# Kernel optimization log

Hardware: AMD Instinct MI355X
Metric: run time of the kernel (lower is better)

## Reference

```python
import jax, jax.numpy as jnp
import numpy as np

N = 100000   # nodes
E = 1600000  # edges
G = 1000     # graphs
S = 32       # state_dim
H = 128      # hidden_dim_message / hidden_dim_output
F = 1        # num_features (edge coulomb)
ROUNDS = 5
NEG_SLOPE = 0.01
LN_EPS = 1e-5


def _ln(x, g, b):
    m = jnp.mean(x, axis=-1, keepdims=True)
    v = jnp.var(x, axis=-1, keepdims=True)
    return (x - m) / jnp.sqrt(v + LN_EPS) * g + b


def _lrelu(x):
    return jnp.where(x >= 0, x, NEG_SLOPE * x)


def _kaiming(k, shape):
    # torch kaiming_normal_(mode='fan_out', nonlinearity='leaky_relu'); W stored [in,out]
    gain = np.sqrt(2.0 / (1.0 + NEG_SLOPE ** 2))
    std = gain / np.sqrt(shape[1])
    return jax.random.normal(k, shape, dtype=jnp.float32) * std


def setup_inputs() -> dict:
    key = jax.random.key(0)
    ks = jax.random.split(key, 10)
    return {
        'node_from': jax.random.randint(ks[0], (E,), 0, N),
        'node_to': jax.random.randint(ks[1], (E,), 0, N),
        'edge_coulomb': jax.random.normal(ks[2], (E, F), dtype=jnp.float32),
        'node_graph_index': jax.random.randint(ks[3], (N,), 0, G),
        'num_nodes': N,
        'num_graphs': G,
        # message_net params
        'W1': _kaiming(ks[4], (S + F, H)), 'b1': jnp.zeros((H,), jnp.float32),
        'g1': jnp.ones((H,), jnp.float32), 'be1': jnp.zeros((H,), jnp.float32),
        'W2': _kaiming(ks[5], (H, S)), 'b2': jnp.zeros((S,), jnp.float32),
        'g2': jnp.ones((S,), jnp.float32), 'be2': jnp.zeros((S,), jnp.float32),
        # output_net params
        'Wo1': _kaiming(ks[6], (S, H)), 'bo1': jnp.zeros((H,), jnp.float32),
        'go': jnp.ones((H,), jnp.float32), 'beo': jnp.zeros((H,), jnp.float32),
        'Wo2': _kaiming(ks[7], (H, 2)), 'bo2': jnp.zeros((2,), jnp.float32),
    }


def reference(node_from, node_to, edge_coulomb, node_graph_index, num_nodes, num_graphs,
              W1, b1, g1, be1, W2, b2, g2, be2, Wo1, bo1, go, beo, Wo2, bo2):
    state = jnp.zeros((num_nodes, S), dtype=edge_coulomb.dtype)
    for _ in range(ROUNDS):
        inp = jnp.concatenate([state[node_from], edge_coulomb], axis=1)  # [E, S+F]
        h = _lrelu(_ln(inp @ W1 + b1, g1, be1))                           # [E, H]
        msg = _lrelu(_ln(h @ W2 + b2, g2, be2))                           # [E, S]
        state = state + jax.ops.segment_sum(msg, node_to, num_segments=num_nodes)
    graph_state = jax.ops.segment_sum(state, node_graph_index, num_segments=num_graphs)  # [G, S]
    h = _lrelu(_ln(graph_state @ Wo1 + bo1, go, beo))
    ev = h @ Wo2 + bo2                                                    # [G, 2]
    mu = ev[:, :1]
    var = jax.nn.softplus(ev[:, 1:])
    return jnp.concatenate([mu, var], axis=1)
```

## Files before the change

kernel.cpp:

```cpp
#include <hip/hip_runtime.h>
#include <hip/hip_bf16.h>

#define NN 100000
#define NE 1600000
#define NG 1000
#define SS 32
#define HH 128
#define ROUNDS 5

constexpr float NEG = 0.01f;
constexpr float EPS = 1e-5f;

constexpr long al4(long x)  { return (x + 3) & ~3L; }
constexpr long al16(long x) { return (x + 15) & ~15L; }

constexpr long OFF_STATE = 0;
constexpr long OFF_GS    = OFF_STATE + (long)NN * SS;
constexpr long OFF_W1T   = OFF_GS + (long)NG * SS;
constexpr long OFF_B1    = OFF_W1T + HH * 33;
constexpr long OFF_G1    = OFF_B1 + HH;
constexpr long OFF_BE1   = OFF_G1 + HH;
constexpr long OFF_W2    = OFF_BE1 + HH;
constexpr long OFF_B2    = OFF_W2 + HH * SS;
constexpr long OFF_G2    = OFF_B2 + SS;
constexpr long OFF_BE2   = OFF_G2 + SS;
constexpr long OFF_WO1   = OFF_BE2 + SS;
constexpr long OFF_BO1   = OFF_WO1 + SS * HH;
constexpr long OFF_GO    = OFF_BO1 + HH;
constexpr long OFF_BEO   = OFF_GO + HH;
constexpr long OFF_WO2   = OFF_BEO + HH;
constexpr long OFF_BO2   = OFF_WO2 + HH * 2;
constexpr long OFF_W1L   = al4(OFF_BO2 + 2);
constexpr long OFF_WSC   = OFF_W1L + HH;
constexpr long OFF_W1B   = al4(OFF_WSC + 2);
constexpr long OFF_W2F   = OFF_W1B + 2048;
constexpr long OFF_WPK   = OFF_W2F + 2048;
constexpr long OFF_Z0P   = OFF_WPK + 192;
constexpr long W_END     = OFF_Z0P + 68;
constexpr long OFF_DELTA = al4(W_END);
constexpr long F_Z      = al4(W_END);
constexpr long F_DEG    = al4(F_Z + (long)NN * 68);
constexpr long F_START  = F_DEG + NN;
constexpr long F_CURSOR = F_START + NN + 4;
constexpr long F_SDEG   = F_CURSOR + NN;
constexpr long F_SSTART = F_SDEG + NN;
constexpr long F_SCUR   = F_SSTART + NN + 4;
constexpr long F_BSUM   = F_SCUR + NN;
constexpr long F_GDEG   = F_BSUM + 512;
constexpr long F_GSTART = F_GDEG + NG;
constexpr long F_GCUR   = F_GSTART + NG + 4;
constexpr long F_GLIST  = F_GCUR + NG;
constexpr long F_EPK    = al16(F_GLIST + NN);
constexpr long F_MSG    = al16(F_EPK + (long)NE * 4);
constexpr long F_RC     = F_MSG;
constexpr long WS_TOTAL = F_MSG + (long)NE * 16;
constexpr long WS_FALLBACK = OFF_DELTA + (long)NN * SS;
constexpr int  NBLK_N  = (NN + 255) / 256;
constexpr int  CHSHIFT = 18;
constexpr int  NCH     = (NE + (1 << CHSHIFT) - 1) >> CHSHIFT;

typedef float f32x4 __attribute__((ext_vector_type(4)));
typedef unsigned int u32x4 __attribute__((ext_vector_type(4)));
typedef short s16x8 __attribute__((ext_vector_type(8)));

__device__ __forceinline__ s16x8 as_s16x8(u32x4 u) {
    union { u32x4 a; s16x8 b; } c; c.a = u; return c.b;
}
__device__ __forceinline__ float bf2f(unsigned short u) {
    union { unsigned int i; float f; } v;
    v.i = ((unsigned int)u) << 16;
    return v.f;
}
__device__ __forceinline__ float lo_bf(unsigned int p) {
    union { unsigned int i; float f; } v; v.i = p << 16; return v.f;
}
__device__ __forceinline__ float hi_bf(unsigned int p) {
    union { unsigned int i; float f; } v; v.i = p & 0xFFFF0000u; return v.f;
}
__device__ __forceinline__ unsigned short f2bf(float f) {
    union { float f; unsigned int u; } x; x.f = f;
    return (unsigned short)((x.u + 0x7FFFu + ((x.u >> 16) & 1u)) >> 16);
}
__device__ __forceinline__ unsigned int pack_bf2(float a, float b) {
    return (unsigned int)f2bf(a) | ((unsigned int)f2bf(b) << 16);
}
#if defined(__has_builtin)
#if __has_builtin(__builtin_amdgcn_cvt_pk_bf16_f32)
#define HAVE_CVT_PK_BF16 1
#endif
#endif
__device__ __forceinline__ unsigned int cvt2bf(float a, float b) {
#ifdef HAVE_CVT_PK_BF16
    auto r = __builtin_amdgcn_cvt_pk_bf16_f32(a, b);
    unsigned int u; __builtin_memcpy(&u, &r, 4); return u;
#else
    return pack_bf2(a, b);
#endif
}
template <int CTRL>
__device__ __forceinline__ float ror_add(float x) {
    int v = __builtin_amdgcn_update_dpp(0, __float_as_int(x), CTRL, 0xF, 0xF, true);
    return x + __int_as_float(v);
}
__device__ __forceinline__ float row_reduce16(float x) {
    x = ror_add<0x121>(x);
    x = ror_add<0x122>(x);
    x = ror_add<0x124>(x);
    x = ror_add<0x128>(x);
    return x;
}
__device__ __forceinline__ int is_bf16(const void* g1raw) {
    return (((const unsigned int*)g1raw)[0] & 0xFFFFu) != 0u;
}
__device__ __forceinline__ float ldf(const void* p, long idx, int bf) {
    return bf ? bf2f(((const unsigned short*)p)[idx]) : ((const float*)p)[idx];
}

__global__ void prep_kernel(
    const void* __restrict__ W1,  const void* __restrict__ b1,
    const void* __restrict__ g1,  const void* __restrict__ be1,
    const void* __restrict__ W2,  const void* __restrict__ b2,
    const void* __restrict__ g2,  const void* __restrict__ be2,
    const void* __restrict__ Wo1, const void* __restrict__ bo1,
    const void* __restrict__ go,  const void* __restrict__ beo,
    const void* __restrict__ Wo2, const void* __restrict__ bo2,
    float* __restrict__ ws)
{
    const int bf = is_bf16(g1);
    long idx = (long)blockIdx.x * blockDim.x + threadIdx.x;
    if (idx < (long)NN * SS) { ws[OFF_STATE + idx] = 0.f; ws[OFF_DELTA + idx] = 0.f; }
    if (idx < (long)NG * SS) ws[OFF_GS + idx] = 0.f;
    if (idx < NN) { ((int*)(ws + F_DEG))[idx] = 0; ((int*)(ws + F_SDEG))[idx] = 0; }
    if (idx < NG) ((int*)(ws + F_GDEG))[idx] = 0;
    if (idx < 33 * HH) {
        int i = (int)(idx / HH), k = (int)(idx % HH);
        ws[OFF_W1T + (long)k * 33 + i] = ldf(W1, idx, bf);
    }
    if (idx < HH) {
        ws[OFF_B1  + idx] = ldf(b1,  idx, bf);
        ws[OFF_G1  + idx] = ldf(g1,  idx, bf);
        ws[OFF_BE1 + idx] = ldf(be1, idx, bf);
        ws[OFF_BO1 + idx] = ldf(bo1, idx, bf);
        ws[OFF_GO  + idx] = ldf(go,  idx, bf);
        ws[OFF_BEO + idx] = ldf(beo, idx, bf);
        ws[OFF_W1L + idx] = ldf(W1, (long)32 * HH + idx, bf);
    }
    if (idx == 0) {
        float sw = 0.f, sq = 0.f;
        float sb = 0.f, qb = 0.f, db = 0.f;
        for (int i = 0; i < HH; i++) {
            float w = ldf(W1, (long)32 * HH + i, bf);
            float x = ldf(b1, i, bf);
            sw += w; sq = fmaf(w, w, sq);
            sb += x; qb = fmaf(x, x, qb); db = fmaf(x, w, db);
        }
        ws[OFF_WSC] = sw; ws[OFF_WSC + 1] = sq;
        float* z0s = ws + OFF_Z0P + 64;
        z0s[0] = sb; z0s[1] = qb; z0s[2] = db; z0s[3] = 0.f;
    }
    if (idx < 64) {
        ((unsigned int*)(ws + OFF_Z0P))[idx] =
            cvt2bf(ldf(b1, 2 * idx, bf), ldf(b1, 2 * idx + 1, bf));
    }
    if (idx < HH * SS) ws[OFF_W2 + idx] = ldf(W2, idx, bf);
    if (idx < SS) {
        ws[OFF_B2  + idx] = ldf(b2,  idx, bf);
        ws[OFF_G2  + idx] = ldf(g2,  idx, bf);
        ws[OFF_BE2 + idx] = ldf(be2, idx, bf);
    }
    if (idx < SS * HH) ws[OFF_WO1 + idx] = ldf(Wo1, idx, bf);
    if (idx < HH * 2)  ws[OFF_WO2 + idx] = ldf(Wo2, idx, bf);
    if (idx < 2)       ws[OFF_BO2 + idx] = ldf(bo2, idx, bf);
    if (idx < 2048) {
        int w = (int)idx;
        int qq = w & 3, L = (w >> 2) & 63, t = (int)(w >> 8);
        int k0 = (L >> 4) * 8 + 2 * qq;
        int n  = t * 16 + (L & 15);
        ((unsigned int*)(ws + OFF_W1B))[w] =
            pack_bf2(ldf(W1, (long)k0 * HH + n, bf), ldf(W1, (long)(k0 + 1) * HH + n, bf));
    }
    if (idx < 2048) {
        int w = (int)idx;
        int qq = w & 3, L = (w >> 2) & 63, t2 = (w >> 8) & 1, ks = (int)(w >> 9);
        int k0 = ks * 32 + (L >> 4) * 8 + 2 * qq;
        int n  = t2 * 16 + (L & 15);
        float v0 = ldf(W2, (long)k0 * SS + n, bf);
        float v1 = ldf(W2, (long)(k0 + 1) * SS + n, bf);
        ((unsigned int*)(ws + OFF_W2F))[w] = pack_bf2(v0, v1);
    }
    if (idx < 192) {
        int w = (int)idx;
        int grp = w / 12, rem = w % 12, slot = rem >> 2, q = rem & 3;
        int ks = grp >> 2, quad = grp & 3;
        int n = ks * 32 + quad * 8 + 2 * q;
        float v0, v1;
        if (slot == 0)      { v0 = ldf(W1, (long)32 * HH + n, bf); v1 = ldf(W1, (long)32 * HH + n + 1, bf); }
        else if (slot == 1) { v0 = ldf(g1, n, bf);  v1 = ldf(g1, n + 1, bf); }
        else                { v0 = ldf(be1, n, bf); v1 = ldf(be1, n + 1, bf); }
        ((unsigned int*)(ws + OFF_WPK))[w] = pack_bf2(v0, v1);
    }
}

__global__ void hist2_kernel(const int* __restrict__ nto, const int* __restrict__ nfrom,
                             float* ws) {
    int e = blockIdx.x * 256 + threadIdx.x;
    if (e < NE) {
        atomicAdd(&((int*)(ws + F_DEG))[nto[e]], 1);
        atomicAdd(&((int*)(ws + F_SDEG))[nfrom[e]], 1);
    }
}

__global__ void scan1_kernel(float* ws, long degOff, long startOff) {
    __shared__ int sh[256];
    int* deg   = (int*)(ws + degOff);
    int* start = (int*)(ws + startOff);
    int* bsum  = (int*)(ws + F_BSUM);
    int i = blockIdx.x * 256 + threadIdx.x;
    int x = (i < NN) ? deg[i] : 0;
    sh[threadIdx.x] = x;
    __syncthreads();
    for (int off = 1; off < 256; off <<= 1) {
        int t = (threadIdx.x >= off) ? sh[threadIdx.x - off] : 0;
        __syncthreads();
        sh[threadIdx.x] += t;
        __syncthreads();
    }
    int incl = sh[threadIdx.x];
    if (i < NN) start[i] = incl - x;
    if (threadIdx.x == 255) bsum[blockIdx.x] = incl;
}

__global__ void scan2p_kernel(float* ws) {
    __shared__ int sh[512];
    int* bsum = (int*)(ws + F_BSUM);
    int t = threadIdx.x;
    int x = (t < NBLK_N) ? bsum[t] : 0;
    sh[t] = x;
    __syncthreads();
    for (int off = 1; off < 512; off <<= 1) {
        int v = (t >= off) ? sh[t - off] : 0;
        __syncthreads();
        sh[t] += v;
        __syncthreads();
    }
    if (t < NBLK_N) bsum[t] = sh[t] - x;
}

__global__ void scan3_kernel(float* ws, long startOff, long curOff) {
    int* start  = (int*)(ws + startOff);
    int* cursor = (int*)(ws + curOff);
    int* bsum   = (int*)(ws + F_BSUM);
    int i = blockIdx.x * 256 + threadIdx.x;
    if (i < NN) {
        int s = start[i] + bsum[i >> 8];
        start[i] = s;
        cursor[i] = s;
        if (i == 0) start[NN] = NE;
    }
}

__global__ void fillseq_kernel(const int* __restrict__ nfrom, const int* __restrict__ nto,
                               const void* __restrict__ ec, const void* __restrict__ g1raw,
                               float* ws) {
    int e = blockIdx.x * 256 + threadIdx.x;
    if (e < NE) {
        int u = nfrom[e];
        int v = nto[e];
        float ecv = ldf(ec, e, is_bf16(g1raw));
        int dpos = atomicAdd(&((int*)(ws + F_CURSOR))[v], 1);
        int spos = atomicAdd(&((int*)(ws + F_SCUR))[u], 1);
        union { float f; unsigned int i; } c; c.f = ecv;
        u32x4 o; o[0] = (unsigned int)u; o[1] = c.i; o[2] = (unsigned int)dpos; o[3] = (unsigned int)spos;
        *(u32x4*)((unsigned int*)(ws + F_RC) + (long)e * 4) = o;
    }
}

__global__ void fillsc_kernel(float* ws, int chunk) {
    int e = blockIdx.x * 256 + threadIdx.x;
    if (e < NE) {
        u32x4 rc = *(const u32x4*)((const unsigned int*)(ws + F_RC) + (long)e * 4);
        if ((int)(rc[3] >> CHSHIFT) == chunk) {
            u32x4 o; o[0] = rc[0]; o[1] = rc[1]; o[2] = rc[2]; o[3] = 0u;
            *(u32x4*)((unsigned int*)(ws + F_EPK) + (long)rc[3] * 4) = o;
        }
    }
}

__global__ void ghist_kernel(const int* __restrict__ gidx, float* ws) {
    int i = blockIdx.x * 256 + threadIdx.x;
    if (i < NN) atomicAdd(&((int*)(ws + F_GDEG))[gidx[i]], 1);
}

__global__ void gscan_kernel(float* ws) {
    __shared__ int sh[1024];
    int* deg   = (int*)(ws + F_GDEG);
    int* start = (int*)(ws + F_GSTART);
    int* cur   = (int*)(ws + F_GCUR);
    int t = threadIdx.x;
    int x = (t < NG) ? deg[t] : 0;
    sh[t] = x;
    __syncthreads();
    for (int off = 1; off < 1024; off <<= 1) {
        int v = (t >= off) ? sh[t - off] : 0;
        __syncthreads();
        sh[t] += v;
        __syncthreads();
    }
    if (t < NG) { start[t] = sh[t] - x; cur[t] = sh[t] - x; }
    if (t == 0) start[NG] = NN;
}

__global__ void gfill_kernel(const int* __restrict__ gidx, float* ws) {
    int i = blockIdx.x * 256 + threadIdx.x;
    if (i < NN) {
        int pos = atomicAdd(&((int*)(ws + F_GCUR))[gidx[i]], 1);
        ((int*)(ws + F_GLIST))[pos] = i;
    }
}

__global__ void z0_kernel(float* __restrict__ ws)
{
    long idx = (long)blockIdx.x * 256 + threadIdx.x;
    if (idx < (long)NN * 68) {
        int slot = (int)(idx % 68);
        ((unsigned int*)(ws + F_Z))[idx] = ((const unsigned int*)(ws + OFF_Z0P))[slot];
    }
}

__launch_bounds__(256)
__global__ void node_kernel(float* __restrict__ ws, int do_z)
{
    __shared__ unsigned short zl[4][16 * 136];
    __shared__ float stl[64 * 33];
    const long nbase = (long)blockIdx.x * 64;

    {
        int t = threadIdx.x;
        int vl = t >> 2, sub = t & 3;
        long v = nbase + vl;
        if (v < NN) {
            const int* start = (const int*)(ws + F_START);
            const u32x4* mb = (const u32x4*)(ws + F_MSG);
            int s0 = start[v], s1 = start[v + 1];
            float* st = ws + OFF_STATE + v * SS + sub * 8;
            float a0 = st[0], a1 = st[1], a2 = st[2], a3 = st[3];
            float a4 = st[4], a5 = st[5], a6 = st[6], a7 = st[7];
            for (int p = s0; p < s1; ++p) {
                u32x4 m = mb[(long)p * 4 + sub];
                a0 += lo_bf(m[0]); a1 += hi_bf(m[0]);
                a2 += lo_bf(m[1]); a3 += hi_bf(m[1]);
                a4 += lo_bf(m[2]); a5 += hi_bf(m[2]);
                a6 += lo_bf(m[3]); a7 += hi_bf(m[3]);
            }
            st[0] = a0; st[1] = a1; st[2] = a2; st[3] = a3;
            st[4] = a4; st[5] = a5; st[6] = a6; st[7] = a7;
            float* sl = stl + vl * 33 + sub * 8;
            sl[0] = a0; sl[1] = a1; sl[2] = a2; sl[3] = a3;
            sl[4] = a4; sl[5] = a5; sl[6] = a6; sl[7] = a7;
        }
    }
    if (!do_z) return;
    __syncthreads();

    const int wv = threadIdx.x >> 6, lane = threadIdx.x & 63;
    const int col = lane & 15, quad = lane >> 4;
    const long vbase = nbase + wv * 16;
    if (vbase >= NN) return;

    const float* sl = stl + (wv * 16 + col) * 33 + quad * 8;
    float st[8];
#pragma unroll
    for (int j = 0; j < 8; j++) st[j] = sl[j];

    u32x4 au;
    au[0] = cvt2bf(st[0], st[1]);
    au[1] = cvt2bf(st[2], st[3]);
    au[2] = cvt2bf(st[4], st[5]);
    au[3] = cvt2bf(st[6], st[7]);
    s16x8 af = as_s16x8(au);

    const u32x4* W1B = (const u32x4*)(ws + OFF_W1B);
    const float* B1 = ws + OFF_B1;
    f32x4 acc[8];
#pragma unroll
    for (int t = 0; t < 8; t++) {
        float bb = B1[t * 16 + col];
        acc[t][0] = bb; acc[t][1] = bb; acc[t][2] = bb; acc[t][3] = bb;
        acc[t] = __builtin_amdgcn_mfma_f32_16x16x32_bf16(af, as_s16x8(W1B[t * 64 + lane]), acc[t], 0, 0, 0);
    }

    float s[4] = {0.f, 0.f, 0.f, 0.f}, q[4] = {0.f, 0.f, 0.f, 0.f}, d[4] = {0.f, 0.f, 0.f, 0.f};
    const float* W1L = ws + OFF_W1L;
#pragma unroll
    for (int t = 0; t < 8; t++) {
        float wl = W1L[t * 16 + col];
#pragma unroll
        for (int r = 0; r < 4; r++) {
            float z = acc[t][r];
            s[r] += z; q[r] = fmaf(z, z, q[r]); d[r] = fmaf(z, wl, d[r]);
        }
    }
#pragma unroll
    for (int r = 0; r < 4; r++) {
        float sr = row_reduce16(s[r]);
        float qr = row_reduce16(q[r]);
        float dr = row_reduce16(d[r]);
        if (col == 0) {
            f32x4 o; o[0] = sr; o[1] = qr; o[2] = dr; o[3] = 0.f;
            *(f32x4*)(ws + F_Z + (vbase + quad * 4 + r) * 68 + 64) = o;
        }
    }

    unsigned short* zw_ = zl[wv];
#pragma unroll
    for (int t = 0; t < 8; t++) {
        unsigned int p01 = cvt2bf(acc[t][0], acc[t][1]);
        unsigned int p23 = cvt2bf(acc[t][2], acc[t][3]);
        unsigned short* b = zw_ + quad * (4 * 136) + t * 16 + col;
        b[0]       = (unsigned short)p01;
        b[136]     = (unsigned short)(p01 >> 16);
        b[2 * 136] = (unsigned short)p23;
        b[3 * 136] = (unsigned short)(p23 >> 16);
    }
    unsigned int* zg = (unsigned int*)(ws + F_Z);
#pragma unroll
    for (int it = 0; it < 4; it++) {
        int byte = it * 1024 + lane * 16;
        int node = byte >> 8;
        int ko   = (byte & 255) >> 2;
        u32x4 val = *(const u32x4*)(zw_ + node * 136 + ((byte & 255) >> 1));
        *(u32x4*)(zg + (vbase + node) * 68L + ko) = val;
    }
}

__launch_bounds__(256)
__global__ void edge_src_kernel(float* __restrict__ ws)
{
    const int lane = threadIdx.x & 63, wv = threadIdx.x >> 6;
    const int col = lane & 15, quad = lane >> 4;

    const u32x4* W2Fp = (const u32x4*)(ws + OFF_W2F);
    u32x4 w2f[8];
#pragma unroll
    for (int i = 0; i < 8; i++) w2f[i] = W2Fp[i * 64 + lane];
    u32x4 wlp[4], gp[4], bep[4];
    const u32x4* WPKp = (const u32x4*)(ws + OFF_WPK);
#pragma unroll
    for (int ks = 0; ks < 4; ks++) {
        const u32x4* W = WPKp + (ks * 4 + quad) * 3;
        wlp[ks] = W[0]; gp[ks] = W[1]; bep[ks] = W[2];
    }
    f32x4 g2h[2], be2h[2], b2h[2];
#pragma unroll
    for (int t2 = 0; t2 < 2; t2++) {
        g2h[t2]  = *(const f32x4*)(ws + OFF_G2  + t2 * 16 + quad * 4);
        be2h[t2] = *(const f32x4*)(ws + OFF_BE2 + t2 * 16 + quad * 4);
        b2h[t2]  = *(const f32x4*)(ws + OFF_B2  + t2 * 16 + quad * 4);
    }
    const float sw1 = ws[OFF_WSC], sqw1 = ws[OFF_WSC + 1];

    const u32x4* EPKp = (const u32x4*)(ws + F_EPK);
    const long tbase = ((long)blockIdx.x * 4 + wv) * 2;

#pragma unroll
    for (int k = 0; k < 2; k++) {
        const int epos = (int)((tbase + k) * 16) + col;
        u32x4 epk = EPKp[epos];
        const int u = (int)epk[0];
        union { unsigned int i; float f; } cc; cc.i = epk[1];
        const float ecv = cc.f;
        const int dsl = (int)epk[2];

        const long zbase = (long)u * 68;
        f32x4 zst = *(const f32x4*)(ws + F_Z + zbase + 64);
        float sumh = fmaf(ecv, sw1, zst[0]);
        float sqh  = fmaf(ecv, fmaf(ecv, sqw1, 2.f * zst[2]), zst[1]);
        float mean = sumh * (1.f / HH);
        float var  = fmaxf(sqh * (1.f / HH) - mean * mean, 0.f);
        float inv  = rsqrtf(var + EPS);
        const float alpha = inv, beta = -mean * inv;

        f32x4 acc2[2];
        acc2[0] = b2h[0]; acc2[1] = b2h[1];

        const unsigned int* zrow = (const unsigned int*)(ws + F_Z) + zbase;
#pragma unroll
        for (int ks = 0; ks < 4; ks++) {
            u32x4 zwv = *(const u32x4*)(zrow + ks * 16 + quad * 4);
            u32x4 hu;
#pragma unroll
            for (int w = 0; w < 4; w++) {
                float z0 = lo_bf(zwv[w]), z1 = hi_bf(zwv[w]);
                float h0 = fmaf(ecv, lo_bf(wlp[ks][w]), z0);
                float h1 = fmaf(ecv, hi_bf(wlp[ks][w]), z1);
                h0 = fmaf(h0, alpha, beta);
                h1 = fmaf(h1, alpha, beta);
                h0 = fmaf(h0, lo_bf(gp[ks][w]), lo_bf(bep[ks][w]));
                h1 = fmaf(h1, hi_bf(gp[ks][w]), hi_bf(bep[ks][w]));
                h0 = fmaxf(h0, NEG * h0);
                h1 = fmaxf(h1, NEG * h1);
                hu[w] = cvt2bf(h0, h1);
            }
            s16x8 hf = as_s16x8(hu);
            acc2[0] = __builtin_amdgcn_mfma_f32_16x16x32_bf16(as_s16x8(w2f[ks * 2 + 0]), hf, acc2[0], 0, 0, 0);
            acc2[1] = __builtin_amdgcn_mfma_f32_16x16x32_bf16(as_s16x8(w2f[ks * 2 + 1]), hf, acc2[1], 0, 0, 0);
        }

        float s2 = 0.f, q2 = 0.f;
#pragma unroll
        for (int t2 = 0; t2 < 2; t2++)
#pragma unroll
            for (int r = 0; r < 4; r++) { float vv = acc2[t2][r]; s2 += vv; q2 = fmaf(vv, vv, q2); }
        s2 += __shfl_xor(s2, 16); q2 += __shfl_xor(q2, 16);
        s2 += __shfl_xor(s2, 32); q2 += __shfl_xor(q2, 32);
        float mean2 = s2 * (1.f / SS);
        float var2  = fmaxf(q2 * (1.f / SS) - mean2 * mean2, 0.f);
        float inv2  = rsqrtf(var2 + EPS);
        const float a2 = inv2, b2c = -mean2 * inv2;

        unsigned int* dst = (unsigned int*)(ws + F_MSG) + (long)dsl * 16;
#pragma unroll
        for (int t2 = 0; t2 < 2; t2++) {
            float m0 = fmaf(fmaf(acc2[t2][0], a2, b2c), g2h[t2][0], be2h[t2][0]);
            float m1 = fmaf(fmaf(acc2[t2][1], a2, b2c), g2h[t2][1], be2h[t2][1]);
            float m2 = fmaf(fmaf(acc2[t2][2], a2, b2c), g2h[t2][2], be2h[t2][2]);
            float m3 = fmaf(fmaf(acc2[t2][3], a2, b2c), g2h[t2][3], be2h[t2][3]);
            m0 = fmaxf(m0, NEG * m0); m1 = fmaxf(m1, NEG * m1);
            m2 = fmaxf(m2, NEG * m2); m3 = fmaxf(m3, NEG * m3);
            uint2 o; o.x = cvt2bf(m0, m1); o.y = cvt2bf(m2, m3);
            *(uint2*)(dst + t2 * 8 + quad * 2) = o;
        }
    }
}

__launch_bounds__(256)
__global__ void graph_gather_kernel(float* __restrict__ ws)
{
    int t = blockIdx.x * 256 + threadIdx.x;
    int g = t >> 5;
    if (g >= NG) return;
    int j = t & 31;
    const int* start = (const int*)(ws + F_GSTART);
    const int* list  = (const int*)(ws + F_GLIST);
    int s0 = start[g], s1 = start[g + 1];
    float acc = 0.f;
    for (int p = s0; p < s1; ++p)
        acc += ws[OFF_STATE + (long)list[p] * SS + j];
    ws[OFF_GS + (long)g * SS + j] = acc;
}

__launch_bounds__(256)
__global__ void edge_atomic_kernel(const int* __restrict__ nfrom, const int* __restrict__ nto,
                                   const void* __restrict__ ec, const void* __restrict__ g1raw,
                                   const float* __restrict__ cws, float* delta)
{
    int e = blockIdx.x * 256 + threadIdx.x;
    if (e >= NE) return;
    const float* state = cws + OFF_STATE;
    const float* W1T = cws + OFF_W1T;
    const float* B1  = cws + OFF_B1;
    const float* G1  = cws + OFF_G1;
    const float* BE1 = cws + OFF_BE1;
    const float* W2  = cws + OFF_W2;
    const float* B2  = cws + OFF_B2;
    const float* G2  = cws + OFF_G2;
    const float* BE2 = cws + OFF_BE2;
    int u = nfrom[e];
    float inp[33];
    const float4* srow = (const float4*)(state + (long)u * SS);
#pragma unroll
    for (int i = 0; i < 8; i++) {
        float4 v = srow[i];
        inp[i * 4 + 0] = v.x; inp[i * 4 + 1] = v.y;
        inp[i * 4 + 2] = v.z; inp[i * 4 + 3] = v.w;
    }
    inp[32] = ldf(ec, e, is_bf16(g1raw));
    float sum = 0.f, sq = 0.f;
    for (int k = 0; k < HH; k++) {
        const float* wr = W1T + k * 33;
        float a = B1[k];
#pragma unroll
        for (int i = 0; i < 33; i++) a = fmaf(inp[i], wr[i], a);
        sum += a; sq = fmaf(a, a, sq);
    }
    float mean = sum * (1.f / HH);
    float var  = sq * (1.f / HH) - mean * mean;
    float inv  = rsqrtf(var + EPS);
    float msg[SS];
#pragma unroll
    for (int j = 0; j < SS; j++) msg[j] = B2[j];
    for (int k = 0; k < HH; k++) {
        const float* wr = W1T + k * 33;
        float a = B1[k];
#pragma unroll
        for (int i = 0; i < 33; i++) a = fmaf(inp[i], wr[i], a);
        float hk = fmaf((a - mean) * inv, G1[k], BE1[k]);
        hk = hk >= 0.f ? hk : NEG * hk;
        const float* w2r = W2 + k * SS;
#pragma unroll
        for (int j = 0; j < SS; j++) msg[j] = fmaf(hk, w2r[j], msg[j]);
    }
    float s2 = 0.f, q2 = 0.f;
#pragma unroll
    for (int j = 0; j < SS; j++) { s2 += msg[j]; q2 = fmaf(msg[j], msg[j], q2); }
    float m2 = s2 * (1.f / SS);
    float v2 = q2 * (1.f / SS) - m2 * m2;
    float i2 = rsqrtf(v2 + EPS);
    int v = nto[e];
    float* drow = delta + (long)v * SS;
#pragma unroll
    for (int j = 0; j < SS; j++) {
        float mj = fmaf((msg[j] - m2) * i2, G2[j], BE2[j]);
        mj = mj >= 0.f ? mj : NEG * mj;
        atomicAdd(drow + j, mj);
    }
}

__global__ void update_kernel(float* ws)
{
    long idx = (long)blockIdx.x * blockDim.x + threadIdx.x;
    if (idx < (long)NN * SS) {
        ws[OFF_STATE + idx] += ws[OFF_DELTA + idx];
        ws[OFF_DELTA + idx] = 0.f;
    }
}

__global__ void graph_kernel(const int* __restrict__ gidx, float* ws)
{
    long idx = (long)blockIdx.x * blockDim.x + threadIdx.x;
    if (idx < (long)NN * SS) {
        int i = (int)(idx >> 5);
        int j = (int)(idx & 31);
        atomicAdd(&ws[OFF_GS + (long)gidx[i] * SS + j], ws[OFF_STATE + idx]);
    }
}

__global__ void readout_kernel(const float* __restrict__ ws, const void* __restrict__ g1raw,
                               void* __restrict__ out)
{
    int g = blockIdx.x;
    int j = threadIdx.x;
    __shared__ float row[SS];
    __shared__ float buf[HH];
    __shared__ float p0[HH];
    __shared__ float p1[HH];

    const float* gs  = ws + OFF_GS;
    const float* Wo1 = ws + OFF_WO1;
    if (j < SS) row[j] = gs[(long)g * SS + j];
    __syncthreads();

    float a = ws[OFF_BO1 + j];
#pragma unroll
    for (int i = 0; i < SS; i++) a = fmaf(row[i], Wo1[i * HH + j], a);
    buf[j] = a;
    __syncthreads();

    float sum = 0.f, sq = 0.f;
    for (int i = 0; i < HH; i++) { float x = buf[i]; sum += x; sq = fmaf(x, x, sq); }
    float mean = sum * (1.f / HH);
    float var  = sq * (1.f / HH) - mean * mean;
    float inv  = rsqrtf(var + EPS);
    float h = fmaf((a - mean) * inv, ws[OFF_GO + j], ws[OFF_BEO + j]);
    h = h >= 0.f ? h : NEG * h;

    p0[j] = h * ws[OFF_WO2 + j * 2 + 0];
    p1[j] = h * ws[OFF_WO2 + j * 2 + 1];
    __syncthreads();

    if (j == 0) {
        float e0 = ws[OFF_BO2 + 0], e1 = ws[OFF_BO2 + 1];
        for (int i = 0; i < HH; i++) { e0 += p0[i]; e1 += p1[i]; }
        float sp = (e1 > 20.f) ? e1 : log1pf(expf(e1));
        if (is_bf16(g1raw)) {
            __hip_bfloat16* o = (__hip_bfloat16*)out;
            o[g * 2 + 0] = __float2bfloat16(e0);
            o[g * 2 + 1] = __float2bfloat16(sp);
        } else {
            float* o = (float*)out;
            o[g * 2 + 0] = e0;
            o[g * 2 + 1] = sp;
        }
    }
}

extern "C" void kernel_launch(void* const* d_in, const int* in_sizes, int n_in,
                              void* d_out, int out_size, void* d_ws, size_t ws_size,
                              hipStream_t stream)
{
    const int* nfrom = (const int*)d_in[0];
    const int* nto   = (const int*)d_in[1];
    const void* ec   = d_in[2];
    const int* gidx  = (const int*)d_in[3];
    const void* W1  = d_in[6];
    const void* b1  = d_in[7];
    const void* g1  = d_in[8];
    const void* be1 = d_in[9];
    const void* W2  = d_in[10];
    const void* b2  = d_in[11];
    const void* g2  = d_in[12];
    const void* be2 = d_in[13];
    const void* Wo1 = d_in[14];
    const void* bo1 = d_in[15];
    const void* go  = d_in[16];
    const void* beo = d_in[17];
    const void* Wo2 = d_in[18];
    const void* bo2 = d_in[19];

    float* ws = (float*)d_ws;
    if (ws_size < (size_t)WS_FALLBACK * sizeof(float)) return;
    const bool gather = ws_size >= (size_t)WS_TOTAL * sizeof(float);

    const int nsBlocks = (int)(((long)NN * SS + 255) / 256);
    const int eBlocks  = (NE + 255) / 256;
    const int efBlocks = NE / 128;
    const int ndBlocks = (NN + 63) / 64;
    const int z0Blocks = (int)(((long)NN * 68 + 255) / 256);
    const int nBlocks1 = (NN + 255) / 256;

    prep_kernel<<<nsBlocks, 256, 0, stream>>>(W1, b1, g1, be1, W2, b2, g2, be2,
                                              Wo1, bo1, go, beo, Wo2, bo2, ws);
    if (gather) {
        hist2_kernel<<<eBlocks, 256, 0, stream>>>(nto, nfrom, ws);
        scan1_kernel<<<NBLK_N, 256, 0, stream>>>(ws, F_DEG, F_START);
        scan2p_kernel<<<1, 512, 0, stream>>>(ws);
        scan3_kernel<<<NBLK_N, 256, 0, stream>>>(ws, F_START, F_CURSOR);
        scan1_kernel<<<NBLK_N, 256, 0, stream>>>(ws, F_SDEG, F_SSTART);
        scan2p_kernel<<<1, 512, 0, stream>>>(ws);
        scan3_kernel<<<NBLK_N, 256, 0, stream>>>(ws, F_SSTART, F_SCUR);
        fillseq_kernel<<<eBlocks, 256, 0, stream>>>(nfrom, nto, ec, g1, ws);
        for (int c = 0; c < NCH; c++)
            fillsc_kernel<<<eBlocks, 256, 0, stream>>>(ws, c);
        ghist_kernel<<<nBlocks1, 256, 0, stream>>>(gidx, ws);
        gscan_kernel<<<1, 1024, 0, stream>>>(ws);
        gfill_kernel<<<nBlocks1, 256, 0, stream>>>(gidx, ws);
        z0_kernel<<<z0Blocks, 256, 0, stream>>>(ws);
        for (int r = 0; r < ROUNDS; r++) {
            edge_src_kernel<<<efBlocks, 256, 0, stream>>>(ws);
            node_kernel    <<<ndBlocks, 256, 0, stream>>>(ws, (r < ROUNDS - 1) ? 1 : 0);
        }
        graph_gather_kernel<<<(NG * 32 + 255) / 256, 256, 0, stream>>>(ws);
    } else {
        for (int r = 0; r < ROUNDS; r++) {
            edge_atomic_kernel<<<eBlocks, 256, 0, stream>>>(nfrom, nto, ec, g1, ws, ws + OFF_DELTA);
            update_kernel<<<nsBlocks, 256, 0, stream>>>(ws);
        }
        graph_kernel<<<nsBlocks, 256, 0, stream>>>(gidx, ws);
    }
    readout_kernel<<<NG, HH, 0, stream>>>(ws, g1, (void*)d_out);
}
```

Baseline: 1.308 ms.

## Fuse histogram into rank-assignment pass and index messages via permutation array

The separate degree histogram is folded into the fill pass: atomic counters now return per-node ranks, and final positions are computed after the scans as start plus rank. The source-sorted edge pack shrinks from 16 to 8 bytes, and messages are written in source-sorted order. The node gather reads them indirectly through a new dest-to-source permutation array. This removes one full edge pass of atomics and halves edge-pack traffic in every round. In exchange, each round's gather does an extra indirect index load and reads messages in a more scattered pattern.

```diff
diff --git a/kernel.cpp b/kernel.cpp
--- a/kernel.cpp
+++ b/kernel.cpp
@@ -39,11 +39,9 @@
 constexpr long W_END     = OFF_Z0P + 68;
 constexpr long OFF_DELTA = al4(W_END);
 constexpr long F_Z      = al4(W_END);
-constexpr long F_DEG    = al4(F_Z + (long)NN * 68);
-constexpr long F_START  = F_DEG + NN;
+constexpr long F_START  = al4(F_Z + (long)NN * 68);
 constexpr long F_CURSOR = F_START + NN + 4;
-constexpr long F_SDEG   = F_CURSOR + NN;
-constexpr long F_SSTART = F_SDEG + NN;
+constexpr long F_SSTART = F_CURSOR + NN;
 constexpr long F_SCUR   = F_SSTART + NN + 4;
 constexpr long F_BSUM   = F_SCUR + NN;
 constexpr long F_GDEG   = F_BSUM + 512;
@@ -51,13 +49,16 @@
 constexpr long F_GCUR   = F_GSTART + NG + 4;
 constexpr long F_GLIST  = F_GCUR + NG;
 constexpr long F_EPK    = al16(F_GLIST + NN);
-constexpr long F_MSG    = al16(F_EPK + (long)NE * 4);
+constexpr long F_SP     = F_EPK + (long)NE * 2;
+constexpr long F_MSG    = al16(F_SP + NE);
 constexpr long F_RC     = F_MSG;
 constexpr long WS_TOTAL = F_MSG + (long)NE * 16;
 constexpr long WS_FALLBACK = OFF_DELTA + (long)NN * SS;
 constexpr int  NBLK_N  = (NN + 255) / 256;
-constexpr int  CHSHIFT = 18;
-constexpr int  NCH     = (NE + (1 << CHSHIFT) - 1) >> CHSHIFT;
+constexpr int  CHSHIFT_E = 19;
+constexpr int  NCH_E     = (NE + (1 << CHSHIFT_E) - 1) >> CHSHIFT_E;
+constexpr int  CHSHIFT_P = 20;
+constexpr int  NCH_P     = (NE + (1 << CHSHIFT_P) - 1) >> CHSHIFT_P;
 
 typedef float f32x4 __attribute__((ext_vector_type(4)));
 typedef unsigned int u32x4 __attribute__((ext_vector_type(4)));
@@ -130,7 +131,7 @@
     long idx = (long)blockIdx.x * blockDim.x + threadIdx.x;
     if (idx < (long)NN * SS) { ws[OFF_STATE + idx] = 0.f; ws[OFF_DELTA + idx] = 0.f; }
     if (idx < (long)NG * SS) ws[OFF_GS + idx] = 0.f;
-    if (idx < NN) { ((int*)(ws + F_DEG))[idx] = 0; ((int*)(ws + F_SDEG))[idx] = 0; }
+    if (idx < NN) { ((int*)(ws + F_CURSOR))[idx] = 0; ((int*)(ws + F_SCUR))[idx] = 0; }
     if (idx < NG) ((int*)(ws + F_GDEG))[idx] = 0;
     if (idx < 33 * HH) {
         int i = (int)(idx / HH), k = (int)(idx % HH);
@@ -201,12 +202,19 @@
     }
 }
 
-__global__ void hist2_kernel(const int* __restrict__ nto, const int* __restrict__ nfrom,
-                             float* ws) {
+__global__ void fillseq_kernel(const int* __restrict__ nfrom, const int* __restrict__ nto,
+                               const void* __restrict__ ec, const void* __restrict__ g1raw,
+                               float* ws) {
     int e = blockIdx.x * 256 + threadIdx.x;
     if (e < NE) {
-        atomicAdd(&((int*)(ws + F_DEG))[nto[e]], 1);
-        atomicAdd(&((int*)(ws + F_SDEG))[nfrom[e]], 1);
+        int u = nfrom[e];
+        int v = nto[e];
+        float ecv = ldf(ec, e, is_bf16(g1raw));
+        int drank = atomicAdd(&((int*)(ws + F_CURSOR))[v], 1);
+        int srank = atomicAdd(&((int*)(ws + F_SCUR))[u], 1);
+        union { float f; unsigned int i; } c; c.f = ecv;
+        u32x4 o; o[0] = (unsigned int)u; o[1] = c.i; o[2] = (unsigned int)drank; o[3] = (unsigned int)srank;
+        *(u32x4*)((unsigned int*)(ws + F_RC) + (long)e * 4) = o;
     }
 }
 
@@ -246,42 +254,36 @@
     if (t < NBLK_N) bsum[t] = sh[t] - x;
 }
 
-__global__ void scan3_kernel(float* ws, long startOff, long curOff) {
+__global__ void scan3_kernel(float* ws, long startOff) {
     int* start  = (int*)(ws + startOff);
-    int* cursor = (int*)(ws + curOff);
     int* bsum   = (int*)(ws + F_BSUM);
     int i = blockIdx.x * 256 + threadIdx.x;
     if (i < NN) {
-        int s = start[i] + bsum[i >> 8];
-        start[i] = s;
-        cursor[i] = s;
+        start[i] += bsum[i >> 8];
         if (i == 0) start[NN] = NE;
     }
 }
 
-__global__ void fillseq_kernel(const int* __restrict__ nfrom, const int* __restrict__ nto,
-                               const void* __restrict__ ec, const void* __restrict__ g1raw,
-                               float* ws) {
-    int e = blockIdx.x * 256 + threadIdx.x;
-    if (e < NE) {
-        int u = nfrom[e];
-        int v = nto[e];
-        float ecv = ldf(ec, e, is_bf16(g1raw));
-        int dpos = atomicAdd(&((int*)(ws + F_CURSOR))[v], 1);
-        int spos = atomicAdd(&((int*)(ws + F_SCUR))[u], 1);
-        union { float f; unsigned int i; } c; c.f = ecv;
-        u32x4 o; o[0] = (unsigned int)u; o[1] = c.i; o[2] = (unsigned int)dpos; o[3] = (unsigned int)spos;
-        *(u32x4*)((unsigned int*)(ws + F_RC) + (long)e * 4) = o;
-    }
-}
-
-__global__ void fillsc_kernel(float* ws, int chunk) {
+__global__ void epkc_kernel(float* ws, int chunk) {
     int e = blockIdx.x * 256 + threadIdx.x;
     if (e < NE) {
         u32x4 rc = *(const u32x4*)((const unsigned int*)(ws + F_RC) + (long)e * 4);
-        if ((int)(rc[3] >> CHSHIFT) == chunk) {
-            u32x4 o; o[0] = rc[0]; o[1] = rc[1]; o[2] = rc[2]; o[3] = 0u;
-            *(u32x4*)((unsigned int*)(ws + F_EPK) + (long)rc[3] * 4) = o;
+        int spos = ((const int*)(ws + F_SSTART))[rc[0]] + (int)rc[3];
+        if ((spos >> CHSHIFT_E) == chunk) {
+            uint2 o; o.x = rc[0]; o.y = rc[1];
+            *(uint2*)((unsigned int*)(ws + F_EPK) + (long)spos * 2) = o;
+        }
+    }
+}
+
+__global__ void spc_kernel(const int* __restrict__ nto, float* ws, int chunk) {
+    int e = blockIdx.x * 256 + threadIdx.x;
+    if (e < NE) {
+        u32x4 rc = *(const u32x4*)((const unsigned int*)(ws + F_RC) + (long)e * 4);
+        int dpos = ((const int*)(ws + F_START))[nto[e]] + (int)rc[2];
+        if ((dpos >> CHSHIFT_P) == chunk) {
+            int spos = ((const int*)(ws + F_SSTART))[rc[0]] + (int)rc[3];
+            ((int*)(ws + F_SP))[dpos] = spos;
         }
     }
 }
@@ -340,13 +342,15 @@
         long v = nbase + vl;
         if (v < NN) {
             const int* start = (const int*)(ws + F_START);
+            const int* SPp   = (const int*)(ws + F_SP);
             const u32x4* mb = (const u32x4*)(ws + F_MSG);
             int s0 = start[v], s1 = start[v + 1];
             float* st = ws + OFF_STATE + v * SS + sub * 8;
             float a0 = st[0], a1 = st[1], a2 = st[2], a3 = st[3];
             float a4 = st[4], a5 = st[5], a6 = st[6], a7 = st[7];
             for (int p = s0; p < s1; ++p) {
-                u32x4 m = mb[(long)p * 4 + sub];
+                int spv = SPp[p];
+                u32x4 m = mb[(long)spv * 4 + sub];
                 a0 += lo_bf(m[0]); a1 += hi_bf(m[0]);
                 a2 += lo_bf(m[1]); a3 += hi_bf(m[1]);
                 a4 += lo_bf(m[2]); a5 += hi_bf(m[2]);
@@ -459,17 +463,16 @@
     }
     const float sw1 = ws[OFF_WSC], sqw1 = ws[OFF_WSC + 1];
 
-    const u32x4* EPKp = (const u32x4*)(ws + F_EPK);
+    const uint2* EPKp = (const uint2*)((const unsigned int*)(ws + F_EPK));
     const long tbase = ((long)blockIdx.x * 4 + wv) * 2;
 
 #pragma unroll
     for (int k = 0; k < 2; k++) {
         const int epos = (int)((tbase + k) * 16) + col;
-        u32x4 epk = EPKp[epos];
-        const int u = (int)epk[0];
-        union { unsigned int i; float f; } cc; cc.i = epk[1];
+        uint2 epk = EPKp[epos];
+        const int u = (int)epk.x;
+        union { unsigned int i; float f; } cc; cc.i = epk.y;
         const float ecv = cc.f;
-        const int dsl = (int)epk[2];
 
         const long zbase = (long)u * 68;
         f32x4 zst = *(const f32x4*)(ws + F_Z + zbase + 64);
@@ -518,7 +521,7 @@
         float inv2  = rsqrtf(var2 + EPS);
         const float a2 = inv2, b2c = -mean2 * inv2;
 
-        unsigned int* dst = (unsigned int*)(ws + F_MSG) + (long)dsl * 16;
+        unsigned int* dst = (unsigned int*)(ws + F_MSG) + (long)epos * 16;
 #pragma unroll
         for (int t2 = 0; t2 < 2; t2++) {
             float m0 = fmaf(fmaf(acc2[t2][0], a2, b2c), g2h[t2][0], be2h[t2][0]);
@@ -721,16 +724,17 @@
     prep_kernel<<<nsBlocks, 256, 0, stream>>>(W1, b1, g1, be1, W2, b2, g2, be2,
                                               Wo1, bo1, go, beo, Wo2, bo2, ws);
     if (gather) {
-        hist2_kernel<<<eBlocks, 256, 0, stream>>>(nto, nfrom, ws);
-        scan1_kernel<<<NBLK_N, 256, 0, stream>>>(ws, F_DEG, F_START);
+        fillseq_kernel<<<eBlocks, 256, 0, stream>>>(nfrom, nto, ec, g1, ws);
+        scan1_kernel<<<NBLK_N, 256, 0, stream>>>(ws, F_CURSOR, F_START);
         scan2p_kernel<<<1, 512, 0, stream>>>(ws);
-        scan3_kernel<<<NBLK_N, 256, 0, stream>>>(ws, F_START, F_CURSOR);
-        scan1_kernel<<<NBLK_N, 256, 0, stream>>>(ws, F_SDEG, F_SSTART);
+        scan3_kernel<<<NBLK_N, 256, 0, stream>>>(ws, F_START);
+        scan1_kernel<<<NBLK_N, 256, 0, stream>>>(ws, F_SCUR, F_SSTART);
         scan2p_kernel<<<1, 512, 0, stream>>>(ws);
-        scan3_kernel<<<NBLK_N, 256, 0, stream>>>(ws, F_SSTART, F_SCUR);
-        fillseq_kernel<<<eBlocks, 256, 0, stream>>>(nfrom, nto, ec, g1, ws);
-        for (int c = 0; c < NCH; c++)
-            fillsc_kernel<<<eBlocks, 256, 0, stream>>>(ws, c);
+        scan3_kernel<<<NBLK_N, 256, 0, stream>>>(ws, F_SSTART);
+        for (int c = 0; c < NCH_E; c++)
+            epkc_kernel<<<eBlocks, 256, 0, stream>>>(ws, c);
+        for (int c = 0; c < NCH_P; c++)
+            spc_kernel<<<eBlocks, 256, 0, stream>>>(nto, ws, c);
         ghist_kernel<<<nBlocks1, 256, 0, stream>>>(gidx, ws);
         gscan_kernel<<<1, 1024, 0, stream>>>(ws);
         gfill_kernel<<<nBlocks1, 256, 0, stream>>>(gidx, ws);
```

Measured after the change: 1.270 ms. -2.9%, faster.
